# Kernel optimization log

Hardware: AMD Instinct MI355X
Metric: run time of the kernel (lower is better)

## Reference

```python
import jax, jax.numpy as jnp
import numpy as np

N_QUBITS = 4
Q_DEPTH = 6
Q_DELTA = 0.01


def _conv1d(x, w, b):
    # x: (B, Cin, L), w: (Cout, Cin, 3), padding=1
    y = jax.lax.conv_general_dilated(x, w, window_strides=(1,), padding=[(1, 1)],
                                     dimension_numbers=('NCH', 'OIH', 'NCH'))
    return y + b[None, :, None]


def _maxpool2(x):
    B, C, L = x.shape
    return x.reshape(B, C, L // 2, 2).max(axis=-1)


def _take(state, i, axis):
    return jax.lax.index_in_dim(state, i, axis, keepdims=False)


def _apply_ry(state, theta, wire):
    # state: (B, 2, 2, 2, 2); theta: scalar (shared weight) or (B,) (per-sample)
    half = theta * 0.5
    c, s = jnp.cos(half), jnp.sin(half)
    if c.ndim == 1:  # per-sample angles -> broadcast over remaining qubit axes
        c = c.reshape(-1, 1, 1, 1)
        s = s.reshape(-1, 1, 1, 1)
    ax = wire + 1
    s0 = _take(state, 0, ax)
    s1 = _take(state, 1, ax)
    return jnp.stack([c * s0 - s * s1, s * s0 + c * s1], axis=ax)


def _apply_cnot(state, ctrl, tgt):
    cax, tax = ctrl + 1, tgt + 1
    a0 = jax.lax.slice_in_dim(state, 0, 1, axis=cax)
    a1 = jax.lax.slice_in_dim(state, 1, 2, axis=cax)
    return jnp.concatenate([a0, jnp.flip(a1, axis=tax)], axis=cax)


def _quantum_forward(q_in, q_params):
    # Batched 4-qubit state-vector simulation (PennyLane default.qubit semantics,
    # wire 0 = most significant -> axis wire+1 of (B,2,2,2,2) state).
    B = q_in.shape[0]
    # H layer on |0000> -> uniform amplitude 1/4
    state = jnp.full((B, 2, 2, 2, 2), 0.25, dtype=q_in.dtype)
    for w in range(N_QUBITS):
        state = _apply_ry(state, q_in[:, w], w)
    qw = q_params.reshape(Q_DEPTH, N_QUBITS)
    for k in range(Q_DEPTH):
        # entangling layer: CNOT(0,1), CNOT(2,3), then CNOT(1,2)
        state = _apply_cnot(state, 0, 1)
        state = _apply_cnot(state, 2, 3)
        state = _apply_cnot(state, 1, 2)
        for w in range(N_QUBITS):
            state = _apply_ry(state, qw[k, w], w)
    probs = state * state  # real amplitudes throughout (H as initial |+>^n, RY, CNOT)
    zs = [(_take(probs, 0, q + 1) - _take(probs, 1, q + 1)).sum(axis=(1, 2, 3))
          for q in range(N_QUBITS)]
    return jnp.stack(zs, axis=1)  # (B, 4) <Z_q>


def setup_inputs() -> dict:
    key = jax.random.key(0)
    ks = jax.random.split(key, 12)
    B, F = 32768, 64
    FLAT = 64 * (F // 4)  # 1024
    return {
        'x': jax.random.normal(ks[0], (B, F), jnp.float32),
        'conv1_w': jax.random.normal(ks[1], (32, 1, 3), jnp.float32) * 0.3,
        'conv1_b': jax.random.normal(ks[2], (32,), jnp.float32) * 0.05,
        'conv2_w': jax.random.normal(ks[3], (64, 32, 3), jnp.float32) * 0.05,
        'conv2_b': jax.random.normal(ks[4], (64,), jnp.float32) * 0.05,
        'fc_w': jax.random.normal(ks[5], (FLAT, 64), jnp.float32) * (1.0 / np.sqrt(FLAT)),
        'fc_b': jax.random.normal(ks[6], (64,), jnp.float32) * 0.05,
        'pre_w': jax.random.normal(ks[7], (64, N_QUBITS), jnp.float32) * 0.125,
        'pre_b': jax.random.normal(ks[8], (N_QUBITS,), jnp.float32) * 0.05,
        'q_params': Q_DELTA * jax.random.normal(ks[9], (Q_DEPTH * N_QUBITS,), jnp.float32),
        'post_w': jax.random.normal(ks[10], (N_QUBITS, 1), jnp.float32) * 0.5,
        'post_b': jax.random.normal(ks[11], (1,), jnp.float32) * 0.05,
    }


def reference(x, conv1_w, conv1_b, conv2_w, conv2_b, fc_w, fc_b,
              pre_w, pre_b, q_params, post_w, post_b):
    h = x[:, None, :]  # (B, 1, F)
    h = _maxpool2(jax.nn.relu(_conv1d(h, conv1_w, conv1_b)))   # (B, 32, F/2)
    h = _maxpool2(jax.nn.relu(_conv1d(h, conv2_w, conv2_b)))   # (B, 64, F/4)
    h = h.reshape(h.shape[0], -1)                              # (B, 1024)
    h = jax.nn.relu(h @ fc_w + fc_b)                           # (B, 64)
    q_in = jnp.tanh(h @ pre_w + pre_b) * (np.pi / 2.0)         # (B, 4)
    q_out = _quantum_forward(q_in, q_params)                   # (B, 4)
    return jax.nn.sigmoid(q_out @ post_w + post_b)             # (B, 1)
```

## Files before the change

### kernel.cpp

```cpp
#include <hip/hip_runtime.h>
#include <math.h>

typedef unsigned short u16;
typedef unsigned int u32;
typedef __attribute__((ext_vector_type(8))) short bf16x8;
typedef __attribute__((ext_vector_type(4))) float f32x4;
typedef __attribute__((ext_vector_type(2))) float f32x2;

__device__ __forceinline__ u16 f32_to_bf16(float f) {
    u32 u = __float_as_uint(f);
    u32 r = u + 0x7FFFu + ((u >> 16) & 1u);
    return (u16)(r >> 16);
}
__device__ __forceinline__ u32 pack2(u16 a, u16 b) { return (u32)a | ((u32)b << 16); }

__device__ __forceinline__ u32 rne_bits(float f) {
    u32 u = __float_as_uint(f);
    return u + 0x7FFFu + ((u >> 16) & 1u);
}
__device__ __forceinline__ u32 pack_rne(float a, float b) {
    return __builtin_amdgcn_perm(rne_bits(b), rne_bits(a), 0x07060302u);
}

__device__ __forceinline__ float fast_tanh(float x) {
    float e = __expf(2.f * x);
    return 1.f - 2.f / (e + 1.f);
}

template<int STRIDE>
__device__ __forceinline__ void ry_gate(float st[16], float theta) {
    float s, c;
    sincosf(theta * 0.5f, &s, &c);
#pragma unroll
    for (int i = 0; i < 16; ++i) {
        if (i & STRIDE) continue;
        float s0 = st[i], s1 = st[i | STRIDE];
        st[i]          = c * s0 - s * s1;
        st[i | STRIDE] = fmaf(s, s0, c * s1);
    }
}
template<int CS, int TS>
__device__ __forceinline__ void cnot_gate(float st[16]) {
#pragma unroll
    for (int i = 0; i < 16; ++i) {
        if ((i & CS) && !(i & TS)) {
            float tmp = st[i]; st[i] = st[i | TS]; st[i | TS] = tmp;
        }
    }
}

__global__ __launch_bounds__(256) void prep_kernel(
    const float* __restrict__ fcw, const float* __restrict__ w2,
    const float* __restrict__ qp,
    u16* __restrict__ whi, u16* __restrict__ w2b, float* __restrict__ Mg)
{
    const int f  = blockIdx.x;
    const int k0 = threadIdx.x * 4;
    u16 hv[4];
#pragma unroll
    for (int i = 0; i < 4; ++i) {
        int k  = k0 + i;
        int op = k >> 6, oc = k & 63;
        hv[i] = f32_to_bf16(fcw[(size_t)(oc * 16 + op) * 64 + f]);
    }
    *(uint2*)(whi + (size_t)f * 1024 + k0) = make_uint2(pack2(hv[0], hv[1]), pack2(hv[2], hv[3]));

    if (threadIdx.x < 96) {
        const int j  = threadIdx.x;
        const int ic = j / 3, t = j - ic * 3;
        w2b[(t * 64 + f) * 32 + ic] = f32_to_bf16(w2[f * 96 + j]);
    }

    if (blockIdx.x == 0 && threadIdx.x < 16) {
        const int j = threadIdx.x;
        float st[16];
#pragma unroll
        for (int i = 0; i < 16; ++i) st[i] = (i == j) ? 1.f : 0.f;
        for (int k = 0; k < 6; ++k) {
            cnot_gate<8, 4>(st);
            cnot_gate<2, 1>(st);
            cnot_gate<4, 2>(st);
            ry_gate<8>(st, qp[k * 4 + 0]);
            ry_gate<4>(st, qp[k * 4 + 1]);
            ry_gate<2>(st, qp[k * 4 + 2]);
            ry_gate<1>(st, qp[k * 4 + 3]);
        }
#pragma unroll
        for (int i = 0; i < 16; ++i) Mg[i * 16 + j] = st[i];
    }
}

__global__ __launch_bounds__(512, 4) void fused_kernel(
    const float* __restrict__ x,
    const float* __restrict__ w1, const float* __restrict__ b1,
    const u16* __restrict__ w2b, const float* __restrict__ b2,
    const u16* __restrict__ whi,
    const float* __restrict__ fcb,
    const float* __restrict__ prew, const float* __restrict__ preb,
    const float* __restrict__ postw, const float* __restrict__ postb,
    const float* __restrict__ Mg,
    float* __restrict__ out)
{
    __shared__ __align__(16) u16 c1h[16 * 1384];
    __shared__ __align__(16) float part[64 * 20];
    __shared__ float prews[256];
    __shared__ float Ms[16][17];

    const int tid  = threadIdx.x;
    const int bs   = blockIdx.x * 16;
    const int wv   = tid >> 6, lane = tid & 63;
    const int lr   = lane & 15, lq = lane >> 4;

    if (tid < 256) {
        prews[tid] = prew[tid];
        Ms[tid >> 4][tid & 15] = Mg[tid];
    }

    const int s1 = tid >> 5;
    const int pp = tid & 31;
    const float* xb = x + (size_t)(bs + s1) * 64;
    const int j = 2 * pp;
    float xm1 = (j == 0)  ? 0.f : xb[j - 1];
    float x0  = xb[j];
    float x1  = xb[j + 1];
    float xp2 = (j == 62) ? 0.f : xb[j + 2];

    bf16x8 af[3][4];
#pragma unroll
    for (int t = 0; t < 3; ++t)
#pragma unroll
        for (int mt = 0; mt < 4; ++mt)
            af[t][mt] = *(const bf16x8*)(w2b + (size_t)(t * 64 + mt * 16 + lr) * 32 + lq * 8);
    f32x4 bias2[4];
#pragma unroll
    for (int mt = 0; mt < 4; ++mt)
        bias2[mt] = *(const f32x4*)(b2 + mt * 16 + lq * 4);

    {
        u16* sbase = c1h + s1 * 1384;
        if (pp == 0 || pp == 31) {
            uint4 z = make_uint4(0, 0, 0, 0);
            uint4* zr = (uint4*)(sbase + (pp == 0 ? 0 : 33) * 40);
            zr[0] = z; zr[1] = z; zr[2] = z; zr[3] = z;
        }
        const f32x2 A1 = {xm1, x0};
        const f32x2 A2 = {x0,  x1};
        const f32x2 A3 = {x1,  xp2};
        u32 row[16];
#pragma unroll
        for (int icp = 0; icp < 16; ++icp) {
            float v[2];
#pragma unroll
            for (int h2 = 0; h2 < 2; ++h2) {
                int ic = icp * 2 + h2;
                float wa = w1[ic * 3], wb = w1[ic * 3 + 1], wc = w1[ic * 3 + 2], bb = b1[ic];
                f32x2 Y = {bb, bb};
                Y += wa * A1;
                Y += wb * A2;
                Y += wc * A3;
                v[h2] = fmaxf(fmaxf(Y.x, Y.y), 0.f);
            }
            row[icp] = pack_rne(v[0], v[1]);
        }
        uint4* d = (uint4*)(sbase + (1 + pp) * 40);
        d[0] = make_uint4(row[0],  row[1],  row[2],  row[3]);
        d[1] = make_uint4(row[4],  row[5],  row[6],  row[7]);
        d[2] = make_uint4(row[8],  row[9],  row[10], row[11]);
        d[3] = make_uint4(row[12], row[13], row[14], row[15]);
    }

#pragma unroll
    for (int nt = 0; nt < 4; ++nt) {
        const int s  = wv * 2 + (nt >> 1);
        const int qb = (nt & 1) * 16;
        const u16* bp = c1h + s * 1384 + (qb + lr) * 40 + lq * 8;
        bf16x8 bf0 = *(const bf16x8*)(bp);
        bf16x8 bf1 = *(const bf16x8*)(bp + 40);
        bf16x8 bf2 = *(const bf16x8*)(bp + 80);
        const int op = (qb + lr) >> 1;
#pragma unroll
        for (int mt = 0; mt < 4; ++mt) {
            f32x4 acc = __builtin_amdgcn_mfma_f32_16x16x32_bf16(af[0][mt], bf0, bias2[mt], 0, 0, 0);
            acc = __builtin_amdgcn_mfma_f32_16x16x32_bf16(af[1][mt], bf1, acc, 0, 0, 0);
            acc = __builtin_amdgcn_mfma_f32_16x16x32_bf16(af[2][mt], bf2, acc, 0, 0, 0);
            float p0 = fmaxf(fmaxf(acc[0], __shfl_xor(acc[0], 1)), 0.f);
            float p1 = fmaxf(fmaxf(acc[1], __shfl_xor(acc[1], 1)), 0.f);
            float p2 = fmaxf(fmaxf(acc[2], __shfl_xor(acc[2], 1)), 0.f);
            float p3 = fmaxf(fmaxf(acc[3], __shfl_xor(acc[3], 1)), 0.f);
            if (!(lane & 1)) {
                *(uint2*)(c1h + s * 1384 + op * 72 + mt * 16 + lq * 4) =
                    make_uint2(pack_rne(p0, p1), pack_rne(p2, p3));
            }
        }
    }
    __syncthreads();

    const int g  = wv & 3;
    const int hf = wv >> 2;
    const int n0 = g * 16;
    f32x4 acc0 = {0.f, 0.f, 0.f, 0.f};
    {
        const u16* ab0 = c1h + (size_t)lr * 1384 + lq * 8;
        const u16* bh0 = whi + (size_t)(n0 + lr) * 1024 + hf * 16 * 32 + lq * 8;
#pragma unroll 8
        for (int i = 0; i < 16; ++i) {
            const int kc = hf * 16 + i;
            const int aoff = (kc >> 1) * 72 + (kc & 1) * 32;
            bf16x8 a0 = *(const bf16x8*)(ab0 + aoff);
            bf16x8 f0 = *(const bf16x8*)(bh0 + i * 32);
            acc0 = __builtin_amdgcn_mfma_f32_16x16x32_bf16(a0, f0, acc0, 0, 0, 0);
        }
    }
    if (hf == 1) {
        *(f32x4*)(part + (n0 + lr) * 20 + lq * 4) = acc0;
    }
    __syncthreads();
    if (hf == 0) {
        const f32x4 pr = *(const f32x4*)(part + (n0 + lr) * 20 + lq * 4);
        const float fb0 = fcb[n0 + lr];
#pragma unroll
        for (int r = 0; r < 4; ++r) {
            float* h0 = (float*)(c1h + (size_t)(lq * 4 + r) * 1384 + 1152);
            h0[n0 + lr] = fmaxf(acc0[r] + pr[r] + fb0, 0.f);
        }
    }
    __syncthreads();

    if (wv == 0) {
        const int L = lane & 3;
        const int s = lane >> 2;
        const float* hfl = (const float*)(c1h + (size_t)s * 1384 + 1152);

        float a0 = 0.f, a1 = 0.f, a2 = 0.f, a3 = 0.f;
#pragma unroll
        for (int i2 = 0; i2 < 4; ++i2) {
            float4 hv = *(const float4*)(hfl + L * 16 + i2 * 4);
#pragma unroll
            for (int c = 0; c < 4; ++c) {
                int ff = L * 16 + i2 * 4 + c;
                float4 pw = *(const float4*)&prews[ff * 4];
                float hx = (c == 0) ? hv.x : (c == 1) ? hv.y : (c == 2) ? hv.z : hv.w;
                a0 = fmaf(hx, pw.x, a0);
                a1 = fmaf(hx, pw.y, a1);
                a2 = fmaf(hx, pw.z, a2);
                a3 = fmaf(hx, pw.w, a3);
            }
        }
        a0 += __shfl_xor(a0, 1); a0 += __shfl_xor(a0, 2);
        a1 += __shfl_xor(a1, 1); a1 += __shfl_xor(a1, 2);
        a2 += __shfl_xor(a2, 1); a2 += __shfl_xor(a2, 2);
        a3 += __shfl_xor(a3, 1); a3 += __shfl_xor(a3, 2);

        const float HP = 1.5707963267948966f;
        float qin[4] = { fast_tanh(a0 + preb[0]) * HP, fast_tanh(a1 + preb[1]) * HP,
                         fast_tanh(a2 + preb[2]) * HP, fast_tanh(a3 + preb[3]) * HP };

        float va[4], vb[4];
        const float RS = 0.70710678118654752f;
#pragma unroll
        for (int w = 0; w < 4; ++w) {
            float sw, cw;
            __sincosf(qin[w] * 0.5f, &sw, &cw);
            va[w] = (cw - sw) * RS;
            vb[w] = (sw + cw) * RS;
        }
        float sv[16];
#pragma unroll
        for (int jj = 0; jj < 16; ++jj) {
            float t = (jj & 8) ? vb[0] : va[0];
            t *= (jj & 4) ? vb[1] : va[1];
            t *= (jj & 2) ? vb[2] : va[2];
            t *= (jj & 1) ? vb[3] : va[3];
            sv[jj] = t;
        }
        float z0 = 0.f, z1 = 0.f, z2 = 0.f, z3 = 0.f;
#pragma unroll
        for (int rr = 0; rr < 4; ++rr) {
            const int r = L * 4 + rr;
            float m = 0.f;
#pragma unroll
            for (int jj = 0; jj < 16; ++jj) m = fmaf(Ms[r][jj], sv[jj], m);
            float p = m * m;
            z0 += (r & 8) ? -p : p;
            z1 += (r & 4) ? -p : p;
            z2 += (r & 2) ? -p : p;
            z3 += (r & 1) ? -p : p;
        }
        z0 += __shfl_xor(z0, 1); z0 += __shfl_xor(z0, 2);
        z1 += __shfl_xor(z1, 1); z1 += __shfl_xor(z1, 2);
        z2 += __shfl_xor(z2, 1); z2 += __shfl_xor(z2, 2);
        z3 += __shfl_xor(z3, 1); z3 += __shfl_xor(z3, 2);

        if (L == 0) {
            float t = postb[0] + z0 * postw[0] + z1 * postw[1] + z2 * postw[2] + z3 * postw[3];
            out[bs + s] = 1.f / (1.f + __expf(-t));
        }
    }
}

extern "C" void kernel_launch(void* const* d_in, const int* in_sizes, int n_in,
                              void* d_out, int out_size, void* d_ws, size_t ws_size,
                              hipStream_t stream) {
    const float* x     = (const float*)d_in[0];
    const float* w1    = (const float*)d_in[1];
    const float* b1    = (const float*)d_in[2];
    const float* w2    = (const float*)d_in[3];
    const float* b2    = (const float*)d_in[4];
    const float* fcw   = (const float*)d_in[5];
    const float* fcb   = (const float*)d_in[6];
    const float* prew  = (const float*)d_in[7];
    const float* preb  = (const float*)d_in[8];
    const float* qp    = (const float*)d_in[9];
    const float* postw = (const float*)d_in[10];
    const float* postb = (const float*)d_in[11];
    float* out = (float*)d_out;

    u16*   fwhi = (u16*)d_ws;
    float* Mg   = (float*)((char*)d_ws + 131072);
    u16*   w2b  = (u16*)((char*)d_ws + 132096);

    const int B = in_sizes[0] / 64;

    prep_kernel<<<dim3(64), dim3(256), 0, stream>>>(fcw, w2, qp, fwhi, w2b, Mg);
    fused_kernel<<<dim3(B / 16), dim3(512), 0, stream>>>(x, w1, b1, w2b, b2,
                                                         fwhi, fcb, prew, preb,
                                                         postw, postb, Mg, out);
}
```

Before: 136.2 us.

## Double block size to 1024 threads, splitting conv1, conv2 and FC work finer

Raises the fused kernel's block from 512 to 1024 threads, which halves the work per thread at each stage. Two threads now compute conv1 for each position, each wave does one sample's conv2 MFMA tiles, and the FC K-reduction is split four ways with three partial buffers combined in shared memory. The aim is more parallelism and latency hiding per block of 16 samples. The cost is more shared memory, more partial-sum traffic, and possibly lower occupancy, since launch_bounds(1024,4) limits registers per thread.

```diff
diff --git a/kernel.cpp b/kernel.cpp
--- a/kernel.cpp
+++ b/kernel.cpp
@@ -90,7 +90,7 @@
     }
 }
 
-__global__ __launch_bounds__(512, 4) void fused_kernel(
+__global__ __launch_bounds__(1024, 4) void fused_kernel(
     const float* __restrict__ x,
     const float* __restrict__ w1, const float* __restrict__ b1,
     const u16* __restrict__ w2b, const float* __restrict__ b2,
@@ -102,7 +102,8 @@
     float* __restrict__ out)
 {
     __shared__ __align__(16) u16 c1h[16 * 1384];
-    __shared__ __align__(16) float part[64 * 20];
+    __shared__ __align__(16) float part3[3 * 1280];
+    __shared__ __align__(16) float hflb[16 * 68];
     __shared__ float prews[256];
     __shared__ float Ms[16][17];
 
@@ -116,8 +117,10 @@
         Ms[tid >> 4][tid & 15] = Mg[tid];
     }
 
-    const int s1 = tid >> 5;
-    const int pp = tid & 31;
+    const int s1   = tid >> 6;
+    const int th   = tid & 63;
+    const int pp   = th & 31;
+    const int half = th >> 5;
     const float* xb = x + (size_t)(bs + s1) * 64;
     const int j = 2 * pp;
     float xm1 = (j == 0)  ? 0.f : xb[j - 1];
@@ -138,7 +141,7 @@
 
     {
         u16* sbase = c1h + s1 * 1384;
-        if (pp == 0 || pp == 31) {
+        if (half == 0 && (pp == 0 || pp == 31)) {
             uint4 z = make_uint4(0, 0, 0, 0);
             uint4* zr = (uint4*)(sbase + (pp == 0 ? 0 : 33) * 40);
             zr[0] = z; zr[1] = z; zr[2] = z; zr[3] = z;
@@ -146,13 +149,13 @@
         const f32x2 A1 = {xm1, x0};
         const f32x2 A2 = {x0,  x1};
         const f32x2 A3 = {x1,  xp2};
-        u32 row[16];
-#pragma unroll
-        for (int icp = 0; icp < 16; ++icp) {
+        u32 row[8];
+#pragma unroll
+        for (int icp = 0; icp < 8; ++icp) {
             float v[2];
 #pragma unroll
             for (int h2 = 0; h2 < 2; ++h2) {
-                int ic = icp * 2 + h2;
+                int ic = (half * 8 + icp) * 2 + h2;
                 float wa = w1[ic * 3], wb = w1[ic * 3 + 1], wc = w1[ic * 3 + 2], bb = b1[ic];
                 f32x2 Y = {bb, bb};
                 Y += wa * A1;
@@ -162,17 +165,15 @@
             }
             row[icp] = pack_rne(v[0], v[1]);
         }
-        uint4* d = (uint4*)(sbase + (1 + pp) * 40);
-        d[0] = make_uint4(row[0],  row[1],  row[2],  row[3]);
-        d[1] = make_uint4(row[4],  row[5],  row[6],  row[7]);
-        d[2] = make_uint4(row[8],  row[9],  row[10], row[11]);
-        d[3] = make_uint4(row[12], row[13], row[14], row[15]);
-    }
-
-#pragma unroll
-    for (int nt = 0; nt < 4; ++nt) {
-        const int s  = wv * 2 + (nt >> 1);
-        const int qb = (nt & 1) * 16;
+        uint4* d = (uint4*)(sbase + (1 + pp) * 40 + half * 16);
+        d[0] = make_uint4(row[0], row[1], row[2], row[3]);
+        d[1] = make_uint4(row[4], row[5], row[6], row[7]);
+    }
+
+#pragma unroll
+    for (int nt = 0; nt < 2; ++nt) {
+        const int s  = wv;
+        const int qb = nt * 16;
         const u16* bp = c1h + s * 1384 + (qb + lr) * 40 + lq * 8;
         bf16x8 bf0 = *(const bf16x8*)(bp);
         bf16x8 bf1 = *(const bf16x8*)(bp + 40);
@@ -196,32 +197,34 @@
     __syncthreads();
 
     const int g  = wv & 3;
-    const int hf = wv >> 2;
+    const int hq = wv >> 2;
     const int n0 = g * 16;
     f32x4 acc0 = {0.f, 0.f, 0.f, 0.f};
     {
         const u16* ab0 = c1h + (size_t)lr * 1384 + lq * 8;
-        const u16* bh0 = whi + (size_t)(n0 + lr) * 1024 + hf * 16 * 32 + lq * 8;
-#pragma unroll 8
-        for (int i = 0; i < 16; ++i) {
-            const int kc = hf * 16 + i;
+        const u16* bh0 = whi + (size_t)(n0 + lr) * 1024 + hq * 8 * 32 + lq * 8;
+#pragma unroll
+        for (int i = 0; i < 8; ++i) {
+            const int kc = hq * 8 + i;
             const int aoff = (kc >> 1) * 72 + (kc & 1) * 32;
             bf16x8 a0 = *(const bf16x8*)(ab0 + aoff);
             bf16x8 f0 = *(const bf16x8*)(bh0 + i * 32);
             acc0 = __builtin_amdgcn_mfma_f32_16x16x32_bf16(a0, f0, acc0, 0, 0, 0);
         }
     }
-    if (hf == 1) {
-        *(f32x4*)(part + (n0 + lr) * 20 + lq * 4) = acc0;
+    if (hq) {
+        *(f32x4*)(&part3[(hq - 1) * 1280 + (n0 + lr) * 20 + lq * 4]) = acc0;
     }
     __syncthreads();
-    if (hf == 0) {
-        const f32x4 pr = *(const f32x4*)(part + (n0 + lr) * 20 + lq * 4);
+    if (hq == 0) {
+        const f32x4 p1_ = *(const f32x4*)(&part3[0 * 1280 + (n0 + lr) * 20 + lq * 4]);
+        const f32x4 p2_ = *(const f32x4*)(&part3[1 * 1280 + (n0 + lr) * 20 + lq * 4]);
+        const f32x4 p3_ = *(const f32x4*)(&part3[2 * 1280 + (n0 + lr) * 20 + lq * 4]);
         const float fb0 = fcb[n0 + lr];
 #pragma unroll
         for (int r = 0; r < 4; ++r) {
-            float* h0 = (float*)(c1h + (size_t)(lq * 4 + r) * 1384 + 1152);
-            h0[n0 + lr] = fmaxf(acc0[r] + pr[r] + fb0, 0.f);
+            hflb[(lq * 4 + r) * 68 + n0 + lr] =
+                fmaxf(acc0[r] + p1_[r] + p2_[r] + p3_[r] + fb0, 0.f);
         }
     }
     __syncthreads();
@@ -229,7 +232,7 @@
     if (wv == 0) {
         const int L = lane & 3;
         const int s = lane >> 2;
-        const float* hfl = (const float*)(c1h + (size_t)s * 1384 + 1152);
+        const float* hfl = hflb + s * 68;
 
         float a0 = 0.f, a1 = 0.f, a2 = 0.f, a3 = 0.f;
 #pragma unroll
@@ -322,7 +325,7 @@
     const int B = in_sizes[0] / 64;
 
     prep_kernel<<<dim3(64), dim3(256), 0, stream>>>(fcw, w2, qp, fwhi, w2b, Mg);
-    fused_kernel<<<dim3(B / 16), dim3(512), 0, stream>>>(x, w1, b1, w2b, b2,
-                                                         fwhi, fcb, prew, preb,
-                                                         postw, postb, Mg, out);
-}
+    fused_kernel<<<dim3(B / 16), dim3(1024), 0, stream>>>(x, w1, b1, w2b, b2,
+                                                          fwhi, fcb, prew, preb,
+                                                          postw, postb, Mg, out);
+}
```

Measured after the change: 191.1 us. 40.3% more time.
